# Optimization experiments

Hardware: AMD Instinct MI355X
Metric: run time of the kernel (lower is better)

The kernel has to match this reference:

```python
import jax, jax.numpy as jnp
import numpy as np

B, L, D, H = 2, 2048, 1024, 16
HD = D // H  # head dim = 64


def setup_inputs() -> dict:
    key = jax.random.key(0)
    ks = jax.random.split(key, 6)
    s = 0.02
    return {
        "hidden_states": jax.random.normal(ks[0], (B, L, D), jnp.float32),
        "attention_mask": jnp.zeros((B, 1, 1, L), jnp.float32),
        "Wq": jax.random.normal(ks[1], (D, D), jnp.float32) * s,
        "bq": jnp.zeros((D,), jnp.float32),
        "Wk": jax.random.normal(ks[2], (D, D), jnp.float32) * s,
        "bk": jnp.zeros((D,), jnp.float32),
        "Wv": jax.random.normal(ks[3], (D, D), jnp.float32) * s,
        "bv": jnp.zeros((D,), jnp.float32),
        "Wo": jax.random.normal(ks[4], (D, D), jnp.float32) * s,
        "bo": jnp.zeros((D,), jnp.float32),
    }


def reference(hidden_states, attention_mask, Wq, bq, Wk, bk, Wv, bv, Wo, bo):
    # Linear projections (torch Linear: x @ W.T + b; here W stored as [in,out])
    q = hidden_states @ Wq + bq  # [B,L,D]
    k = hidden_states @ Wk + bk
    v = hidden_states @ Wv + bv

    def split_heads(x):  # [B,L,D] -> [B,H,L,HD]
        return x.reshape(B, L, H, HD).transpose(0, 2, 1, 3)

    q, k, v = split_heads(q), split_heads(k), split_heads(v)

    scores = jnp.einsum("bhqd,bhkd->bhqk", q, k) / jnp.sqrt(
        jnp.asarray(HD, q.dtype)
    )
    scores = scores + attention_mask  # additive mask, broadcast [B,1,1,L]
    pdtype = scores.dtype
    # fp32 upcast around softmax, as in the original module
    probs = jax.nn.softmax(scores.astype(jnp.float32), axis=-1).astype(pdtype)
    # dropout prob = 0 (eval) -> identity; head_mask=None
    ctx = jnp.einsum("bhqk,bhkd->bhqd", probs, v)  # [B,H,L,HD]
    ctx = ctx.transpose(0, 2, 1, 3).reshape(B, L, D)
    out = ctx @ Wo + bo  # BertSelfOutput_preLN dense (dropout=0)
    return out
```

## Files before the change

kernel.cpp:

```cpp
#include <hip/hip_runtime.h>

#define BB 2
#define LL 2048
#define DDIM 1024
#define HH 16
#define HDIM 64
#define MM (BB*LL)
#define KK 1024
#define LOG2E 1.44269504f

typedef __attribute__((ext_vector_type(8))) short s8v;
typedef __attribute__((ext_vector_type(8))) unsigned short u8v;
typedef __attribute__((ext_vector_type(4))) float f4v;
typedef __attribute__((ext_vector_type(16))) float f16v;

__device__ __forceinline__ unsigned short f2bf(float f) {
    unsigned int u = __float_as_uint(f);
    u += 0x7fffu + ((u >> 16) & 1u);
    return (unsigned short)(u >> 16);
}

__device__ __forceinline__ float fexp2(float x) { return __builtin_amdgcn_exp2f(x); }

__device__ __forceinline__ void gld_lds16(const unsigned short* g, unsigned short* l) {
    __builtin_amdgcn_global_load_lds(
        (const __attribute__((address_space(1))) unsigned int*)g,
        (__attribute__((address_space(3))) unsigned int*)l, 16, 0, 0);
}

__global__ __launch_bounds__(256) void prep(
        const float* __restrict__ X,
        const float* __restrict__ Wq, const float* __restrict__ Wk,
        const float* __restrict__ Wv, const float* __restrict__ Wo,
        unsigned short* __restrict__ Xb,
        unsigned short* __restrict__ WqT, unsigned short* __restrict__ WkT,
        unsigned short* __restrict__ WvT, unsigned short* __restrict__ WoT) {
    __shared__ float lds[64][65];
    const int blk = blockIdx.x, t = threadIdx.x;
    if (blk < 4096) {
        int i = blk * 256 + t;
        float4 v = ((const float4*)X)[i];
        ushort4 r;
        r.x = f2bf(v.x); r.y = f2bf(v.y); r.z = f2bf(v.z); r.w = f2bf(v.w);
        ((ushort4*)Xb)[i] = r;
        return;
    }
    const int tb = blk - 4096;
    const int w = tb >> 8;
    const int tile = tb & 255;
    const int k0 = (tile >> 4) * 64, n0 = (tile & 15) * 64;
    const float* src; unsigned short* dst;
    switch (w) {
        case 0: src = Wq; dst = WqT; break;
        case 1: src = Wk; dst = WkT; break;
        case 2: src = Wv; dst = WvT; break;
        default: src = Wo; dst = WoT; break;
    }
    #pragma unroll
    for (int j = 0; j < 4; ++j) {
        int r = (t >> 4) + 16*j, c = (t & 15) * 4;
        float4 v = *(const float4*)(src + (size_t)(k0 + r) * DDIM + n0 + c);
        lds[r][c] = v.x; lds[r][c+1] = v.y; lds[r][c+2] = v.z; lds[r][c+3] = v.w;
    }
    __syncthreads();
    #pragma unroll
    for (int j = 0; j < 2; ++j) {
        int rr = (t >> 3) + 32*j, cc = (t & 7) * 8;
        u8v o;
        #pragma unroll
        for (int i = 0; i < 8; ++i) o[i] = f2bf(lds[cc + i][rr]);
        *(u8v*)(dst + (size_t)(n0 + rr) * KK + k0 + cc) = o;
    }
}

__device__ __forceinline__ void gemm_core(const unsigned short* __restrict__ A,
                                          const unsigned short* __restrict__ BT,
                                          int Mbase, int Nbase,
                                          unsigned short* As, unsigned short* Bs,
                                          f4v acc[4][4]) {
    const int t = threadIdx.x;
    const int lane = t & 63, wave = t >> 6;
    const int wm = wave & 1, wn = wave >> 1;
    const int l15 = lane & 15, quad = lane >> 4;
    const int srow = t >> 2, schunk = (t & 3) * 8;

    #pragma unroll
    for (int mt = 0; mt < 4; ++mt)
        #pragma unroll
        for (int nt = 0; nt < 4; ++nt)
            acc[mt][nt] = f4v{0.f, 0.f, 0.f, 0.f};

    const unsigned short* gA0 = A  + (size_t)(Mbase + srow)      * KK + schunk;
    const unsigned short* gA1 = A  + (size_t)(Mbase + 64 + srow) * KK + schunk;
    const unsigned short* gB0 = BT + (size_t)(Nbase + srow)      * KK + schunk;
    const unsigned short* gB1 = BT + (size_t)(Nbase + 64 + srow) * KK + schunk;
    unsigned short* lA0 = As + t*8;
    unsigned short* lA1 = As + 64*32 + t*8;
    unsigned short* lB0 = Bs + t*8;
    unsigned short* lB1 = Bs + 64*32 + t*8;

    for (int kb = 0; kb < KK; kb += 32) {
        __syncthreads();
        gld_lds16(gA0 + kb, lA0);
        gld_lds16(gA1 + kb, lA1);
        gld_lds16(gB0 + kb, lB0);
        gld_lds16(gB1 + kb, lB1);
        __syncthreads();
        s8v af[4], bfv[4];
        #pragma unroll
        for (int mt = 0; mt < 4; ++mt)
            af[mt] = *(const s8v*)(As + (wm*64 + mt*16 + l15)*32 + quad*8);
        #pragma unroll
        for (int nt = 0; nt < 4; ++nt)
            bfv[nt] = *(const s8v*)(Bs + (wn*64 + nt*16 + l15)*32 + quad*8);
        #pragma unroll
        for (int mt = 0; mt < 4; ++mt)
            #pragma unroll
            for (int nt = 0; nt < 4; ++nt)
                acc[mt][nt] = __builtin_amdgcn_mfma_f32_16x16x32_bf16(af[mt], bfv[nt], acc[mt][nt], 0, 0, 0);
    }
}

__global__ __launch_bounds__(256) void qkv_gemm(
        const unsigned short* __restrict__ Xb,
        const unsigned short* __restrict__ WqT, const unsigned short* __restrict__ WkT,
        const unsigned short* __restrict__ WvT,
        const float* __restrict__ bq, const float* __restrict__ bk, const float* __restrict__ bv,
        unsigned short* __restrict__ Qh, unsigned short* __restrict__ Kh,
        unsigned short* __restrict__ Vt) {
    __shared__ alignas(16) unsigned short As[128*32];
    __shared__ alignas(16) unsigned short Bs[128*32];

    const int n = blockIdx.x;
    const int xcd = n & 7, r = n >> 3;
    const int gx = xcd >> 1, gy = xcd & 1;
    const int mode = r % 3;
    const int r2 = r / 3;
    const int x = gx*2 + (r2 & 1);
    const int y = gy*16 + (r2 >> 1);

    const unsigned short* BT = (mode == 0) ? WqT : (mode == 1) ? WkT : WvT;
    const float* bias        = (mode == 0) ? bq  : (mode == 1) ? bk  : bv;
    unsigned short* out      = (mode == 0) ? Qh  : (mode == 1) ? Kh  : Vt;
    const int Mbase = y * 128, Nbase = x * 128;

    f4v acc[4][4];
    gemm_core(Xb, BT, Mbase, Nbase, As, Bs, acc);

    const int lane = threadIdx.x & 63, wave = threadIdx.x >> 6;
    const int wm = wave & 1, wn = wave >> 1, l15 = lane & 15, quad = lane >> 4;
    #pragma unroll
    for (int mt = 0; mt < 4; ++mt)
        #pragma unroll
        for (int nt = 0; nt < 4; ++nt)
            #pragma unroll
            for (int rr = 0; rr < 4; ++rr) {
                int gm = Mbase + wm*64 + mt*16 + quad*4 + rr;
                int gn = Nbase + wn*64 + nt*16 + l15;
                float v = acc[mt][nt][rr] + bias[gn];
                int bb = gm >> 11, ll = gm & 2047;
                int hh = gn >> 6,  dd = gn & 63;
                if (mode == 2)
                    out[((size_t)(bb*HH + hh)*HDIM + dd)*LL + ll] = f2bf(v);
                else
                    out[((size_t)(bb*HH + hh)*LL + ll)*HDIM + dd] = f2bf(v);
            }
}

__global__ __launch_bounds__(256) void attn(
        const unsigned short* __restrict__ Qh, const unsigned short* __restrict__ Kh,
        const unsigned short* __restrict__ Vt, const float* __restrict__ mask,
        unsigned short* __restrict__ ctx) {
    __shared__ alignas(16) unsigned short Ks[64*72];
    __shared__ alignas(16) unsigned short Vs[64*72];
    __shared__ alignas(16) unsigned short P [4*32*72];

    const int t = threadIdx.x, lane = t & 63, wave = t >> 6;
    const int l31 = lane & 31, hgrp = lane >> 5;

    const int n = blockIdx.x;
    const int bh = (n & 7) * 4 + ((n >> 3) & 3);
    const int qblk = n >> 5;
    const int b = bh >> 4, hh = bh & 15;

    const unsigned short* Qb = Qh + (size_t)bh * LL * HDIM;
    const unsigned short* Kb = Kh + (size_t)bh * LL * HDIM;
    const unsigned short* Vb = Vt + (size_t)bh * HDIM * LL;
    const float* mb = mask + (size_t)b * LL;
    const int q0 = qblk * 128 + wave * 32;
    unsigned short* Pw = P + wave * 32 * 72;

    const int srow = t >> 2, scol = (t & 3) * 16;

    s8v qf[4];
    #pragma unroll
    for (int hf = 0; hf < 4; ++hf)
        qf[hf] = *(const s8v*)(Qb + (size_t)(q0 + l31)*HDIM + hf*16 + hgrp*8);

    f16v o[2];
    #pragma unroll
    for (int nc = 0; nc < 2; ++nc)
        #pragma unroll
        for (int r = 0; r < 16; ++r) o[nc][r] = 0.f;
    float rs[16];
    #pragma unroll
    for (int r = 0; r < 16; ++r) rs[r] = 0.f;

    const float C1 = 0.125f * LOG2E;

    for (int kt = 0; kt < LL; kt += 64) {
        float4 ka  = *(const float4*)(Kb + (size_t)(kt + srow)*HDIM + scol);
        float4 kb2 = *(const float4*)(Kb + (size_t)(kt + srow)*HDIM + scol + 8);
        float4 va  = *(const float4*)(Vb + (size_t)srow*LL + kt + scol);
        float4 vb2 = *(const float4*)(Vb + (size_t)srow*LL + kt + scol + 8);
        float mv0 = mb[kt + l31] * LOG2E;
        float mv1 = mb[kt + 32 + l31] * LOG2E;

        __syncthreads();
        *(float4*)(Ks + srow*72 + scol)     = ka;
        *(float4*)(Ks + srow*72 + scol + 8) = kb2;
        *(float4*)(Vs + srow*72 + scol)     = va;
        *(float4*)(Vs + srow*72 + scol + 8) = vb2;
        __syncthreads();

        f16v sac[2];
        #pragma unroll
        for (int kc = 0; kc < 2; ++kc) {
            #pragma unroll
            for (int r = 0; r < 16; ++r) sac[kc][r] = 0.f;
            #pragma unroll
            for (int hf = 0; hf < 4; ++hf) {
                s8v kf = *(const s8v*)(Ks + (kc*32 + l31)*72 + hf*16 + hgrp*8);
                sac[kc] = __builtin_amdgcn_mfma_f32_32x32x16_bf16(qf[hf], kf, sac[kc], 0, 0, 0);
            }
        }
        #pragma unroll
        for (int kc = 0; kc < 2; ++kc) {
            float mvv = kc ? mv1 : mv0;
            #pragma unroll
            for (int r = 0; r < 16; ++r) {
                float p = fexp2(sac[kc][r] * C1 + mvv);
                rs[r] += p;
                int row = (r & 3) + 8*(r >> 2) + 4*hgrp;
                Pw[row*72 + kc*32 + l31] = (unsigned short)(__float_as_uint(p) >> 16);
            }
        }
        #pragma unroll
        for (int kt16 = 0; kt16 < 4; ++kt16) {
            s8v pf = *(const s8v*)(Pw + l31*72 + kt16*16 + hgrp*8);
            #pragma unroll
            for (int nc = 0; nc < 2; ++nc) {
                s8v vf = *(const s8v*)(Vs + (nc*32 + l31)*72 + kt16*16 + hgrp*8);
                o[nc] = __builtin_amdgcn_mfma_f32_32x32x16_bf16(pf, vf, o[nc], 0, 0, 0);
            }
        }
    }

    #pragma unroll
    for (int r = 0; r < 16; ++r) {
        float s0 = rs[r];
        s0 += __shfl_xor(s0, 1);
        s0 += __shfl_xor(s0, 2);
        s0 += __shfl_xor(s0, 4);
        s0 += __shfl_xor(s0, 8);
        s0 += __shfl_xor(s0, 16);
        rs[r] = 1.0f / s0;
    }
    #pragma unroll
    for (int r = 0; r < 16; ++r) {
        int row = (r & 3) + 8*(r >> 2) + 4*hgrp;
        int q = q0 + row;
        size_t base = ((size_t)b*LL + q)*DDIM + hh*HDIM;
        #pragma unroll
        for (int nc = 0; nc < 2; ++nc)
            ctx[base + nc*32 + l31] = f2bf(o[nc][r] * rs[r]);
    }
}

__global__ __launch_bounds__(256) void out_gemm(
        const unsigned short* __restrict__ Cb, const unsigned short* __restrict__ WoT,
        const float* __restrict__ bo, float* __restrict__ out) {
    __shared__ alignas(16) unsigned short As[128*32];
    __shared__ alignas(16) unsigned short Bs[64*32];
    const int t = threadIdx.x;
    const int lane = t & 63, wave = t >> 6;
    const int wm = wave & 1, wn = wave >> 1;
    const int l15 = lane & 15, quad = lane >> 4;
    const int srow = t >> 2, schunk = (t & 3) * 8;

    const int n = blockIdx.x;
    const int xcd = n & 7, r0 = n >> 3;
    const int x = r0 & 15, ysub = r0 >> 4;
    const int y = ysub * 8 + xcd;
    const int Mbase = y * 128, Nbase = x * 64;

    f4v acc[4][2];
    #pragma unroll
    for (int mt = 0; mt < 4; ++mt)
        #pragma unroll
        for (int nt = 0; nt < 2; ++nt)
            acc[mt][nt] = f4v{0.f, 0.f, 0.f, 0.f};

    const unsigned short* gA0 = Cb  + (size_t)(Mbase + srow)      * KK + schunk;
    const unsigned short* gA1 = Cb  + (size_t)(Mbase + 64 + srow) * KK + schunk;
    const unsigned short* gB0 = WoT + (size_t)(Nbase + srow)      * KK + schunk;
    unsigned short* lA0 = As + t*8;
    unsigned short* lA1 = As + 64*32 + t*8;
    unsigned short* lB0 = Bs + t*8;

    for (int kb = 0; kb < KK; kb += 32) {
        __syncthreads();
        gld_lds16(gA0 + kb, lA0);
        gld_lds16(gA1 + kb, lA1);
        gld_lds16(gB0 + kb, lB0);
        __syncthreads();
        s8v af[4], bfv[2];
        #pragma unroll
        for (int mt = 0; mt < 4; ++mt)
            af[mt] = *(const s8v*)(As + (wm*64 + mt*16 + l15)*32 + quad*8);
        #pragma unroll
        for (int nt = 0; nt < 2; ++nt)
            bfv[nt] = *(const s8v*)(Bs + (wn*32 + nt*16 + l15)*32 + quad*8);
        #pragma unroll
        for (int mt = 0; mt < 4; ++mt)
            #pragma unroll
            for (int nt = 0; nt < 2; ++nt)
                acc[mt][nt] = __builtin_amdgcn_mfma_f32_16x16x32_bf16(af[mt], bfv[nt], acc[mt][nt], 0, 0, 0);
    }

    #pragma unroll
    for (int mt = 0; mt < 4; ++mt)
        #pragma unroll
        for (int nt = 0; nt < 2; ++nt)
            #pragma unroll
            for (int rr = 0; rr < 4; ++rr) {
                int gm = Mbase + wm*64 + mt*16 + quad*4 + rr;
                int gn = Nbase + wn*32 + nt*16 + l15;
                out[(size_t)gm*DDIM + gn] = acc[mt][nt][rr] + bo[gn];
            }
}

extern "C" void kernel_launch(void* const* d_in, const int* in_sizes, int n_in,
                              void* d_out, int out_size, void* d_ws, size_t ws_size,
                              hipStream_t stream) {
    const float* X    = (const float*)d_in[0];
    const float* mask = (const float*)d_in[1];
    const float* Wq   = (const float*)d_in[2];
    const float* bq   = (const float*)d_in[3];
    const float* Wk   = (const float*)d_in[4];
    const float* bk   = (const float*)d_in[5];
    const float* Wv   = (const float*)d_in[6];
    const float* bv   = (const float*)d_in[7];
    const float* Wo   = (const float*)d_in[8];
    const float* bo   = (const float*)d_in[9];
    float* out = (float*)d_out;

    char* ws = (char*)d_ws;
    unsigned short* Xb  = (unsigned short*)(ws);
    unsigned short* WqT = (unsigned short*)(ws + (8u  << 20));
    unsigned short* WkT = (unsigned short*)(ws + (10u << 20));
    unsigned short* WvT = (unsigned short*)(ws + (12u << 20));
    unsigned short* WoT = (unsigned short*)(ws + (14u << 20));
    unsigned short* Qh  = (unsigned short*)(ws + (16u << 20));
    unsigned short* Kh  = (unsigned short*)(ws + (24u << 20));
    unsigned short* Vt  = (unsigned short*)(ws + (32u << 20));
    unsigned short* Cb  = Xb;

    prep     <<<dim3(5120),  dim3(256), 0, stream>>>(X, Wq, Wk, Wv, Wo, Xb, WqT, WkT, WvT, WoT);
    qkv_gemm <<<dim3(768),   dim3(256), 0, stream>>>(Xb, WqT, WkT, WvT, bq, bk, bv, Qh, Kh, Vt);
    attn     <<<dim3(512),   dim3(256), 0, stream>>>(Qh, Kh, Vt, mask, Cb);
    out_gemm <<<dim3(512),   dim3(256), 0, stream>>>(Cb, WoT, bo, out);
}
```

Before: 209.8 us.

## Fuse Q/K/V projections into one block sharing the X tile

```diff
diff --git a/kernel.cpp b/kernel.cpp
--- a/kernel.cpp
+++ b/kernel.cpp
@@ -73,54 +73,6 @@
     }
 }
 
-__device__ __forceinline__ void gemm_core(const unsigned short* __restrict__ A,
-                                          const unsigned short* __restrict__ BT,
-                                          int Mbase, int Nbase,
-                                          unsigned short* As, unsigned short* Bs,
-                                          f4v acc[4][4]) {
-    const int t = threadIdx.x;
-    const int lane = t & 63, wave = t >> 6;
-    const int wm = wave & 1, wn = wave >> 1;
-    const int l15 = lane & 15, quad = lane >> 4;
-    const int srow = t >> 2, schunk = (t & 3) * 8;
-
-    #pragma unroll
-    for (int mt = 0; mt < 4; ++mt)
-        #pragma unroll
-        for (int nt = 0; nt < 4; ++nt)
-            acc[mt][nt] = f4v{0.f, 0.f, 0.f, 0.f};
-
-    const unsigned short* gA0 = A  + (size_t)(Mbase + srow)      * KK + schunk;
-    const unsigned short* gA1 = A  + (size_t)(Mbase + 64 + srow) * KK + schunk;
-    const unsigned short* gB0 = BT + (size_t)(Nbase + srow)      * KK + schunk;
-    const unsigned short* gB1 = BT + (size_t)(Nbase + 64 + srow) * KK + schunk;
-    unsigned short* lA0 = As + t*8;
-    unsigned short* lA1 = As + 64*32 + t*8;
-    unsigned short* lB0 = Bs + t*8;
-    unsigned short* lB1 = Bs + 64*32 + t*8;
-
-    for (int kb = 0; kb < KK; kb += 32) {
-        __syncthreads();
-        gld_lds16(gA0 + kb, lA0);
-        gld_lds16(gA1 + kb, lA1);
-        gld_lds16(gB0 + kb, lB0);
-        gld_lds16(gB1 + kb, lB1);
-        __syncthreads();
-        s8v af[4], bfv[4];
-        #pragma unroll
-        for (int mt = 0; mt < 4; ++mt)
-            af[mt] = *(const s8v*)(As + (wm*64 + mt*16 + l15)*32 + quad*8);
-        #pragma unroll
-        for (int nt = 0; nt < 4; ++nt)
-            bfv[nt] = *(const s8v*)(Bs + (wn*64 + nt*16 + l15)*32 + quad*8);
-        #pragma unroll
-        for (int mt = 0; mt < 4; ++mt)
-            #pragma unroll
-            for (int nt = 0; nt < 4; ++nt)
-                acc[mt][nt] = __builtin_amdgcn_mfma_f32_16x16x32_bf16(af[mt], bfv[nt], acc[mt][nt], 0, 0, 0);
-    }
-}
-
 __global__ __launch_bounds__(256) void qkv_gemm(
         const unsigned short* __restrict__ Xb,
         const unsigned short* __restrict__ WqT, const unsigned short* __restrict__ WkT,
@@ -129,42 +81,86 @@
         unsigned short* __restrict__ Qh, unsigned short* __restrict__ Kh,
         unsigned short* __restrict__ Vt) {
     __shared__ alignas(16) unsigned short As[128*32];
-    __shared__ alignas(16) unsigned short Bs[128*32];
+    __shared__ alignas(16) unsigned short Bs[3][64*32];
+
+    const int t = threadIdx.x;
+    const int lane = t & 63, wave = t >> 6;
+    const int wm = wave & 1, wn = wave >> 1;
+    const int l15 = lane & 15, quad = lane >> 4;
+    const int srow = t >> 2, schunk = (t & 3) * 8;
 
     const int n = blockIdx.x;
-    const int xcd = n & 7, r = n >> 3;
-    const int gx = xcd >> 1, gy = xcd & 1;
-    const int mode = r % 3;
-    const int r2 = r / 3;
-    const int x = gx*2 + (r2 & 1);
-    const int y = gy*16 + (r2 >> 1);
-
-    const unsigned short* BT = (mode == 0) ? WqT : (mode == 1) ? WkT : WvT;
-    const float* bias        = (mode == 0) ? bq  : (mode == 1) ? bk  : bv;
-    unsigned short* out      = (mode == 0) ? Qh  : (mode == 1) ? Kh  : Vt;
-    const int Mbase = y * 128, Nbase = x * 128;
-
-    f4v acc[4][4];
-    gemm_core(Xb, BT, Mbase, Nbase, As, Bs, acc);
-
-    const int lane = threadIdx.x & 63, wave = threadIdx.x >> 6;
-    const int wm = wave & 1, wn = wave >> 1, l15 = lane & 15, quad = lane >> 4;
-    #pragma unroll
-    for (int mt = 0; mt < 4; ++mt)
-        #pragma unroll
-        for (int nt = 0; nt < 4; ++nt)
-            #pragma unroll
-            for (int rr = 0; rr < 4; ++rr) {
-                int gm = Mbase + wm*64 + mt*16 + quad*4 + rr;
-                int gn = Nbase + wn*64 + nt*16 + l15;
-                float v = acc[mt][nt][rr] + bias[gn];
-                int bb = gm >> 11, ll = gm & 2047;
-                int hh = gn >> 6,  dd = gn & 63;
-                if (mode == 2)
-                    out[((size_t)(bb*HH + hh)*HDIM + dd)*LL + ll] = f2bf(v);
-                else
-                    out[((size_t)(bb*HH + hh)*LL + ll)*HDIM + dd] = f2bf(v);
-            }
+    const int xcd = n & 7, x = (n >> 3) & 15, youter = n >> 7;
+    const int y = xcd + 8 * youter;
+    const int Mbase = y * 128, Nbase = x * 64;
+
+    f4v acc[3][4][2];
+    #pragma unroll
+    for (int m = 0; m < 3; ++m)
+        #pragma unroll
+        for (int mt = 0; mt < 4; ++mt)
+            #pragma unroll
+            for (int nt = 0; nt < 2; ++nt)
+                acc[m][mt][nt] = f4v{0.f, 0.f, 0.f, 0.f};
+
+    const unsigned short* gA0 = Xb  + (size_t)(Mbase + srow)      * KK + schunk;
+    const unsigned short* gA1 = Xb  + (size_t)(Mbase + 64 + srow) * KK + schunk;
+    const unsigned short* gBq = WqT + (size_t)(Nbase + srow)      * KK + schunk;
+    const unsigned short* gBk = WkT + (size_t)(Nbase + srow)      * KK + schunk;
+    const unsigned short* gBv = WvT + (size_t)(Nbase + srow)      * KK + schunk;
+    unsigned short* lA0 = As + t*8;
+    unsigned short* lA1 = As + 64*32 + t*8;
+    unsigned short* lB0 = Bs[0] + t*8;
+    unsigned short* lB1 = Bs[1] + t*8;
+    unsigned short* lB2 = Bs[2] + t*8;
+
+    for (int kb = 0; kb < KK; kb += 32) {
+        __syncthreads();
+        gld_lds16(gA0 + kb, lA0);
+        gld_lds16(gA1 + kb, lA1);
+        gld_lds16(gBq + kb, lB0);
+        gld_lds16(gBk + kb, lB1);
+        gld_lds16(gBv + kb, lB2);
+        __syncthreads();
+        s8v af[4], bfv[3][2];
+        #pragma unroll
+        for (int mt = 0; mt < 4; ++mt)
+            af[mt] = *(const s8v*)(As + (wm*64 + mt*16 + l15)*32 + quad*8);
+        #pragma unroll
+        for (int m = 0; m < 3; ++m)
+            #pragma unroll
+            for (int nt = 0; nt < 2; ++nt)
+                bfv[m][nt] = *(const s8v*)(Bs[m] + (wn*32 + nt*16 + l15)*32 + quad*8);
+        #pragma unroll
+        for (int m = 0; m < 3; ++m)
+            #pragma unroll
+            for (int mt = 0; mt < 4; ++mt)
+                #pragma unroll
+                for (int nt = 0; nt < 2; ++nt)
+                    acc[m][mt][nt] = __builtin_amdgcn_mfma_f32_16x16x32_bf16(af[mt], bfv[m][nt], acc[m][mt][nt], 0, 0, 0);
+    }
+
+    #pragma unroll
+    for (int m = 0; m < 3; ++m) {
+        const float* bias   = (m == 0) ? bq : (m == 1) ? bk : bv;
+        unsigned short* out = (m == 0) ? Qh : (m == 1) ? Kh : Vt;
+        #pragma unroll
+        for (int mt = 0; mt < 4; ++mt)
+            #pragma unroll
+            for (int nt = 0; nt < 2; ++nt)
+                #pragma unroll
+                for (int rr = 0; rr < 4; ++rr) {
+                    int gm = Mbase + wm*64 + mt*16 + quad*4 + rr;
+                    int gn = Nbase + wn*32 + nt*16 + l15;
+                    float v = acc[m][mt][nt][rr] + bias[gn];
+                    int bb = gm >> 11, ll = gm & 2047;
+                    int hh = gn >> 6,  dd = gn & 63;
+                    if (m == 2)
+                        out[((size_t)(bb*HH + hh)*HDIM + dd)*LL + ll] = f2bf(v);
+                    else
+                        out[((size_t)(bb*HH + hh)*LL + ll)*HDIM + dd] = f2bf(v);
+                }
+    }
 }
 
 __global__ __launch_bounds__(256) void attn(
@@ -367,7 +363,7 @@
     unsigned short* Cb  = Xb;
 
     prep     <<<dim3(5120),  dim3(256), 0, stream>>>(X, Wq, Wk, Wv, Wo, Xb, WqT, WkT, WvT, WoT);
-    qkv_gemm <<<dim3(768),   dim3(256), 0, stream>>>(Xb, WqT, WkT, WvT, bq, bk, bv, Qh, Kh, Vt);
+    qkv_gemm <<<dim3(512),   dim3(256), 0, stream>>>(Xb, WqT, WkT, WvT, bq, bk, bv, Qh, Kh, Vt);
     attn     <<<dim3(512),   dim3(256), 0, stream>>>(Qh, Kh, Vt, mask, Cb);
     out_gemm <<<dim3(512),   dim3(256), 0, stream>>>(Cb, WoT, bo, out);
 }
```

Measured after the change: 236.5 us. +12.8%, slower.

## Double-buffer K/V tiles in attention kernel to overlap global loads with MFMA

Applied to the files above, without the earlier changes.

```diff
diff --git a/kernel.cpp b/kernel.cpp
--- a/kernel.cpp
+++ b/kernel.cpp
@@ -171,8 +171,7 @@
         const unsigned short* __restrict__ Qh, const unsigned short* __restrict__ Kh,
         const unsigned short* __restrict__ Vt, const float* __restrict__ mask,
         unsigned short* __restrict__ ctx) {
-    __shared__ alignas(16) unsigned short Ks[64*72];
-    __shared__ alignas(16) unsigned short Vs[64*72];
+    __shared__ alignas(16) unsigned short KV[2][2*64*72];
     __shared__ alignas(16) unsigned short P [4*32*72];
 
     const int t = threadIdx.x, lane = t & 63, wave = t >> 6;
@@ -208,20 +207,36 @@
 
     const float C1 = 0.125f * LOG2E;
 
-    for (int kt = 0; kt < LL; kt += 64) {
-        float4 ka  = *(const float4*)(Kb + (size_t)(kt + srow)*HDIM + scol);
-        float4 kb2 = *(const float4*)(Kb + (size_t)(kt + srow)*HDIM + scol + 8);
-        float4 va  = *(const float4*)(Vb + (size_t)srow*LL + kt + scol);
-        float4 vb2 = *(const float4*)(Vb + (size_t)srow*LL + kt + scol + 8);
-        float mv0 = mb[kt + l31] * LOG2E;
-        float mv1 = mb[kt + 32 + l31] * LOG2E;
-
-        __syncthreads();
-        *(float4*)(Ks + srow*72 + scol)     = ka;
-        *(float4*)(Ks + srow*72 + scol + 8) = kb2;
-        *(float4*)(Vs + srow*72 + scol)     = va;
-        *(float4*)(Vs + srow*72 + scol + 8) = vb2;
-        __syncthreads();
+    float4 ka  = *(const float4*)(Kb + (size_t)srow*HDIM + scol);
+    float4 kb2 = *(const float4*)(Kb + (size_t)srow*HDIM + scol + 8);
+    float4 va  = *(const float4*)(Vb + (size_t)srow*LL + scol);
+    float4 vb2 = *(const float4*)(Vb + (size_t)srow*LL + scol + 8);
+    float mvc0 = mb[l31] * LOG2E;
+    float mvc1 = mb[32 + l31] * LOG2E;
+    {
+        unsigned short* Kn = KV[0];
+        unsigned short* Vn = KV[0] + 64*72;
+        *(float4*)(Kn + srow*72 + scol)     = ka;
+        *(float4*)(Kn + srow*72 + scol + 8) = kb2;
+        *(float4*)(Vn + srow*72 + scol)     = va;
+        *(float4*)(Vn + srow*72 + scol + 8) = vb2;
+    }
+    __syncthreads();
+
+    for (int i = 0; i < 32; ++i) {
+        const int kt = i * 64;
+        const unsigned short* Kc = KV[i & 1];
+        const unsigned short* Vc = KV[i & 1] + 64*72;
+
+        float mvn0 = 0.f, mvn1 = 0.f;
+        if (i < 31) {
+            ka  = *(const float4*)(Kb + (size_t)(kt + 64 + srow)*HDIM + scol);
+            kb2 = *(const float4*)(Kb + (size_t)(kt + 64 + srow)*HDIM + scol + 8);
+            va  = *(const float4*)(Vb + (size_t)srow*LL + kt + 64 + scol);
+            vb2 = *(const float4*)(Vb + (size_t)srow*LL + kt + 64 + scol + 8);
+            mvn0 = mb[kt + 64 + l31];
+            mvn1 = mb[kt + 96 + l31];
+        }
 
         f16v sac[2];
         #pragma unroll
@@ -230,13 +245,13 @@
             for (int r = 0; r < 16; ++r) sac[kc][r] = 0.f;
             #pragma unroll
             for (int hf = 0; hf < 4; ++hf) {
-                s8v kf = *(const s8v*)(Ks + (kc*32 + l31)*72 + hf*16 + hgrp*8);
+                s8v kf = *(const s8v*)(Kc + (kc*32 + l31)*72 + hf*16 + hgrp*8);
                 sac[kc] = __builtin_amdgcn_mfma_f32_32x32x16_bf16(qf[hf], kf, sac[kc], 0, 0, 0);
             }
         }
         #pragma unroll
         for (int kc = 0; kc < 2; ++kc) {
-            float mvv = kc ? mv1 : mv0;
+            float mvv = kc ? mvc1 : mvc0;
             #pragma unroll
             for (int r = 0; r < 16; ++r) {
                 float p = fexp2(sac[kc][r] * C1 + mvv);
@@ -250,9 +265,21 @@
             s8v pf = *(const s8v*)(Pw + l31*72 + kt16*16 + hgrp*8);
             #pragma unroll
             for (int nc = 0; nc < 2; ++nc) {
-                s8v vf = *(const s8v*)(Vs + (nc*32 + l31)*72 + kt16*16 + hgrp*8);
+                s8v vf = *(const s8v*)(Vc + (nc*32 + l31)*72 + kt16*16 + hgrp*8);
                 o[nc] = __builtin_amdgcn_mfma_f32_32x32x16_bf16(pf, vf, o[nc], 0, 0, 0);
             }
+        }
+
+        if (i < 31) {
+            unsigned short* Kn = KV[(i + 1) & 1];
+            unsigned short* Vn = KV[(i + 1) & 1] + 64*72;
+            *(float4*)(Kn + srow*72 + scol)     = ka;
+            *(float4*)(Kn + srow*72 + scol + 8) = kb2;
+            *(float4*)(Vn + srow*72 + scol)     = va;
+            *(float4*)(Vn + srow*72 + scol + 8) = vb2;
+            mvc0 = mvn0 * LOG2E;
+            mvc1 = mvn1 * LOG2E;
+            __syncthreads();
         }
     }
 
```

New measurement: 209.3 us. Within noise of the previous version (-0.2%).
